# Kernel optimization log

Hardware: AMD Instinct MI355X
Metric: run time of the kernel (lower is better)

Reference implementation:

```python
import jax, jax.numpy as jnp
import numpy as np

IDIM = 512
HDIM = 1024
CDIM = 128  # part_size; topk uses k = 2*CDIM (share=True)
B, T = 16, 4096


def _multihot(idx, n):
    """idx: [B, T, K] int32 -> [B, T, n] float 0/1 multi-hot.
    Matches one_hot(idx, n).float().sum(-2); topk indices are unique so add==set."""
    b, t, k = idx.shape
    rows = jnp.arange(b * t)[:, None]
    m = jnp.zeros((b * t, n), jnp.float32).at[rows, idx.reshape(-1, k)].add(1.0)
    return m.reshape(b, t, n)


def setup_inputs() -> dict:
    key = jax.random.key(0)
    ks = jax.random.split(key, 12)
    inp = {}
    inp["x"] = jax.random.normal(ks[0], (B, T, IDIM), jnp.float32)
    inp["mask_prev"] = (jax.random.uniform(ks[1], (B, T, HDIM)) < 0.1).astype(jnp.float32)

    def lin(k, i, o):
        return jax.random.normal(k, (i, o), jnp.float32) * (1.0 / np.sqrt(i))

    dims_e = [IDIM, 512, 512, 512, HDIM]
    dims_d = [HDIM, 512, 512, 512, IDIM]
    for i in range(4):
        inp[f"e_w{i}"] = lin(ks[2 + i], dims_e[i], dims_e[i + 1])
        inp[f"e_b{i}"] = jnp.zeros((dims_e[i + 1],), jnp.float32)
        inp[f"d_w{i}"] = lin(ks[6 + i], dims_d[i], dims_d[i + 1])
        inp[f"d_b{i}"] = jnp.zeros((dims_d[i + 1],), jnp.float32)
    return inp


def _mlp(x, ws, bs):
    for w, b in zip(ws[:-1], bs[:-1]):
        x = jax.nn.relu(x @ w + b)
    return x @ ws[-1] + bs[-1]


def reference(x, mask_prev,
              e_w0, e_b0, e_w1, e_b1, e_w2, e_b2, e_w3, e_b3,
              d_w0, d_b0, d_w1, d_b1, d_w2, d_b2, d_w3, d_b3):
    h = _mlp(x, [e_w0, e_w1, e_w2, e_w3], [e_b0, e_b1, e_b2, e_b3])  # [B,T,HDIM]

    # hidden_exclude_activation (mask_prev is not None branch)
    h = jnp.where(mask_prev > 0, jnp.float32(0.0), h)  # h[mask_prev.byte()] = 0
    energy = h * h
    _, idx = jax.lax.top_k(energy, 2 * CDIM)            # sorted desc, like torch.topk
    mask_cur_share = _multihot(idx, HDIM)               # top 2*cdim multi-hot
    # h.masked_fill(~mask_cur_share, 0): keep only the shared top-2*cdim energies
    h = h * mask_cur_share

    # decoder
    out = _mlp(h, [d_w0, d_w1, d_w2, d_w3], [d_b0, d_b1, d_b2, d_b3])  # [B,T,IDIM]
    return out
```

## Files before the change

### kernel.cpp

```cpp
#include <hip/hip_runtime.h>

constexpr int NTOK = 16 * 4096;
constexpr int KSEL = 256;
constexpr int UCAP = 8192;

using short8 = __attribute__((ext_vector_type(8))) short;
using f32x4  = __attribute__((ext_vector_type(4))) float;

__device__ inline unsigned short bf16_rne(float x) {
    unsigned u = __float_as_uint(x);
    unsigned r = u + 0x7fffu + ((u >> 16) & 1u);
    return (unsigned short)(r >> 16);
}
__device__ inline float bf16_f32(unsigned short h) {
    return __uint_as_float((unsigned)h << 16);
}

template<int K>
__global__ __launch_bounds__(256)
void gemm_f32(const float* __restrict__ A, const float* __restrict__ W,
              const float* __restrict__ bias, float* __restrict__ C,
              int M, int do_relu, const float* __restrict__ mask)
{
    __shared__ float sA[16][136];
    __shared__ float sW[16][68];

    const int tid = threadIdx.x;
    const int tx = tid & 15, ty = tid >> 4;
    const int rowBase = blockIdx.y * 128;
    const int colBase = blockIdx.x * 64;

    const int lr = tid >> 1;
    const int lk = (tid & 1) * 8;
    const int wk = tid >> 4;
    const int wc = (tid & 15) * 4;

    float acc[8][4] = {};

    for (int k0 = 0; k0 < K; k0 += 16) {
        const float* ap = &A[(size_t)(rowBase + lr) * K + k0 + lk];
        float4 a0 = *(const float4*)ap;
        float4 a1 = *(const float4*)(ap + 4);
        float4 wv = *(const float4*)&W[(size_t)(k0 + wk) * M + colBase + wc];
        __syncthreads();
        sA[lk + 0][lr] = a0.x; sA[lk + 1][lr] = a0.y;
        sA[lk + 2][lr] = a0.z; sA[lk + 3][lr] = a0.w;
        sA[lk + 4][lr] = a1.x; sA[lk + 5][lr] = a1.y;
        sA[lk + 6][lr] = a1.z; sA[lk + 7][lr] = a1.w;
        *(float4*)&sW[wk][wc] = wv;
        __syncthreads();
#pragma unroll
        for (int k = 0; k < 16; ++k) {
            float4 aA = *(const float4*)&sA[k][ty * 8];
            float4 aB = *(const float4*)&sA[k][ty * 8 + 4];
            float4 w4 = *(const float4*)&sW[k][tx * 4];
            float av[8] = {aA.x, aA.y, aA.z, aA.w, aB.x, aB.y, aB.z, aB.w};
            float wl[4] = {w4.x, w4.y, w4.z, w4.w};
#pragma unroll
            for (int a = 0; a < 8; ++a)
#pragma unroll
                for (int b = 0; b < 4; ++b)
                    acc[a][b] = fmaf(av[a], wl[b], acc[a][b]);
        }
    }

    float4 bv = *(const float4*)&bias[colBase + tx * 4];
    float bb[4] = {bv.x, bv.y, bv.z, bv.w};
#pragma unroll
    for (int a = 0; a < 8; ++a) {
        int row = rowBase + ty * 8 + a;
        float o[4];
#pragma unroll
        for (int b = 0; b < 4; ++b) {
            o[b] = acc[a][b] + bb[b];
            if (do_relu) o[b] = fmaxf(o[b], 0.f);
        }
        if (mask) {
            float4 mv = *(const float4*)&mask[(size_t)row * M + colBase + tx * 4];
            float mm[4] = {mv.x, mv.y, mv.z, mv.w};
#pragma unroll
            for (int b = 0; b < 4; ++b) if (mm[b] > 0.f) o[b] = 0.f;
        }
        float4 ov = {o[0], o[1], o[2], o[3]};
        *(float4*)&C[(size_t)row * M + colBase + tx * 4] = ov;
    }
}

__global__ __launch_bounds__(256)
void wsplit_t(const float* __restrict__ W, unsigned short* __restrict__ WhT,
              unsigned short* __restrict__ WlT, int K, int M)
{
    __shared__ float tile[32][33];
    const int tid = threadIdx.x;
    const int tx = tid & 31, ty = tid >> 5;
    const int m0 = blockIdx.x * 32, k0 = blockIdx.y * 32;
#pragma unroll
    for (int i = 0; i < 4; ++i)
        tile[ty + 8 * i][tx] = W[(size_t)(k0 + ty + 8 * i) * M + m0 + tx];
    __syncthreads();
#pragma unroll
    for (int i = 0; i < 4; ++i) {
        int m = ty + 8 * i;
        float v = tile[tx][m];
        unsigned short hh = bf16_rne(v);
        unsigned short ll = bf16_rne(v - bf16_f32(hh));
        WhT[(size_t)(m0 + m) * K + k0 + tx] = hh;
        WlT[(size_t)(m0 + m) * K + k0 + tx] = ll;
    }
}

template<int K>
__global__ __launch_bounds__(256)
void gemm_mfma(const float* __restrict__ A, const unsigned short* __restrict__ WhT,
               const unsigned short* __restrict__ WlT, const float* __restrict__ bias,
               float* __restrict__ C, int M, int do_relu)
{
    __shared__ __align__(16) unsigned short sAh[128 * 40];
    __shared__ __align__(16) unsigned short sAl[128 * 40];
    __shared__ __align__(16) unsigned short sBh[128 * 40];
    __shared__ __align__(16) unsigned short sBl[128 * 40];

    const int tid = threadIdx.x;
    const int lane = tid & 63, wid = tid >> 6;
    const int quad = lane >> 4, l16 = lane & 15;
    const int rowBase = blockIdx.y * 128, colBase = blockIdx.x * 128;
    const int wr = (wid & 1) * 64, wc = (wid >> 1) * 64;

    const int sr = tid >> 1;
    const int sk = (tid & 1) * 16;

    f32x4 acc[4][4];
#pragma unroll
    for (int i = 0; i < 4; ++i)
#pragma unroll
        for (int j = 0; j < 4; ++j)
            acc[i][j] = (f32x4){0.f, 0.f, 0.f, 0.f};

    for (int k0 = 0; k0 < K; k0 += 32) {
        const float* ap = &A[(size_t)(rowBase + sr) * K + k0 + sk];
        float4 a0 = *(const float4*)ap;
        float4 a1 = *(const float4*)(ap + 4);
        float4 a2 = *(const float4*)(ap + 8);
        float4 a3 = *(const float4*)(ap + 12);
        const unsigned short* whp = &WhT[(size_t)(colBase + sr) * K + k0 + sk];
        const unsigned short* wlp = &WlT[(size_t)(colBase + sr) * K + k0 + sk];
        short8 wh0 = *(const short8*)whp;
        short8 wh1 = *(const short8*)(whp + 8);
        short8 wl0 = *(const short8*)wlp;
        short8 wl1 = *(const short8*)(wlp + 8);

        float f[16] = {a0.x, a0.y, a0.z, a0.w, a1.x, a1.y, a1.z, a1.w,
                       a2.x, a2.y, a2.z, a2.w, a3.x, a3.y, a3.z, a3.w};
        unsigned short __align__(16) hs[16], ls[16];
#pragma unroll
        for (int j = 0; j < 16; ++j) {
            hs[j] = bf16_rne(f[j]);
            ls[j] = bf16_rne(f[j] - bf16_f32(hs[j]));
        }

        __syncthreads();
        *(short8*)&sAh[sr * 40 + sk]     = *(short8*)&hs[0];
        *(short8*)&sAh[sr * 40 + sk + 8] = *(short8*)&hs[8];
        *(short8*)&sAl[sr * 40 + sk]     = *(short8*)&ls[0];
        *(short8*)&sAl[sr * 40 + sk + 8] = *(short8*)&ls[8];
        *(short8*)&sBh[sr * 40 + sk]     = wh0;
        *(short8*)&sBh[sr * 40 + sk + 8] = wh1;
        *(short8*)&sBl[sr * 40 + sk]     = wl0;
        *(short8*)&sBl[sr * 40 + sk + 8] = wl1;
        __syncthreads();

        short8 ah[4], al[4], bh[4], bl[4];
#pragma unroll
        for (int t4 = 0; t4 < 4; ++t4) {
            ah[t4] = *(const short8*)&sAh[(wr + t4 * 16 + l16) * 40 + quad * 8];
            al[t4] = *(const short8*)&sAl[(wr + t4 * 16 + l16) * 40 + quad * 8];
            bh[t4] = *(const short8*)&sBh[(wc + t4 * 16 + l16) * 40 + quad * 8];
            bl[t4] = *(const short8*)&sBl[(wc + t4 * 16 + l16) * 40 + quad * 8];
        }
#pragma unroll
        for (int rt = 0; rt < 4; ++rt)
#pragma unroll
            for (int ct = 0; ct < 4; ++ct) {
                acc[rt][ct] = __builtin_amdgcn_mfma_f32_16x16x32_bf16(ah[rt], bh[ct], acc[rt][ct], 0, 0, 0);
                acc[rt][ct] = __builtin_amdgcn_mfma_f32_16x16x32_bf16(al[rt], bh[ct], acc[rt][ct], 0, 0, 0);
                acc[rt][ct] = __builtin_amdgcn_mfma_f32_16x16x32_bf16(ah[rt], bl[ct], acc[rt][ct], 0, 0, 0);
            }
    }

#pragma unroll
    for (int ct = 0; ct < 4; ++ct) {
        int col = colBase + wc + ct * 16 + l16;
        float bc = bias[col];
#pragma unroll
        for (int rt = 0; rt < 4; ++rt)
#pragma unroll
            for (int r = 0; r < 4; ++r) {
                int row = rowBase + wr + rt * 16 + quad * 4 + r;
                float v = acc[rt][ct][r] + bc;
                if (do_relu) v = fmaxf(v, 0.f);
                C[(size_t)row * M + col] = v;
            }
    }
}

__global__ __launch_bounds__(256)
void topk_pass1(float* __restrict__ h, int* __restrict__ meta)
{
    const int t = blockIdx.x, tid = threadIdx.x;
    const int lane = tid & 63, wid = tid >> 6;

    __shared__ unsigned hist[256];
    __shared__ unsigned wsum[4];
    __shared__ unsigned dmx[4];
    __shared__ unsigned s_prefix;
    __shared__ int s_need;

    float4 hv = ((const float4*)(h + (size_t)t * 1024))[tid];
    float v[4] = {hv.x, hv.y, hv.z, hv.w};
    unsigned u[4];
#pragma unroll
    for (int j = 0; j < 4; ++j) u[j] = __float_as_uint(v[j] * v[j]);

    if (tid == 0) { s_prefix = 0u; s_need = KSEL; }
    __syncthreads();

    for (int p = 3; p >= 0; --p) {
        unsigned pref = s_prefix;
        int need = s_need;
        hist[tid] = 0u;
        __syncthreads();
#pragma unroll
        for (int j = 0; j < 4; ++j) {
            bool match = (p == 3) || ((u[j] >> (8 * (p + 1))) == (pref >> (8 * (p + 1))));
            if (match) atomicAdd(&hist[(u[j] >> (8 * p)) & 255u], 1u);
        }
        __syncthreads();
        unsigned x = hist[tid];
        unsigned s = x;
#pragma unroll
        for (int off = 1; off < 64; off <<= 1) {
            unsigned o = __shfl_down(s, off);
            if (lane + off < 64) s += o;
        }
        if (lane == 0) wsum[wid] = s;
        __syncthreads();
        unsigned above = 0;
        for (int w = wid + 1; w < 4; ++w) above += wsum[w];
        unsigned incl = s + above;
        unsigned excl = incl - x;
        if (incl >= (unsigned)need && excl < (unsigned)need) {
            s_prefix = pref | ((unsigned)tid << (8 * p));
            s_need = need - (int)excl;
        }
        __syncthreads();
    }
    const unsigned tau = s_prefix;

    unsigned cg = 0, ce = 0;
#pragma unroll
    for (int j = 0; j < 4; ++j) {
        cg += (u[j] > tau) ? 1u : 0u;
        ce += (u[j] == tau) ? 1u : 0u;
    }
    unsigned packed = (cg << 16) | ce;
    unsigned ps = packed;
#pragma unroll
    for (int off = 1; off < 64; off <<= 1) {
        unsigned o = __shfl_up(ps, off);
        if (lane >= off) ps += o;
    }
    if (lane == 63) wsum[wid] = ps;
    __syncthreads();
    unsigned below = 0;
    for (int w = 0; w < wid; ++w) below += wsum[w];
    unsigned total = wsum[0] + wsum[1] + wsum[2] + wsum[3];
    unsigned incl = ps + below;
    int need_eq = KSEL - (int)(total >> 16);
    int eq_base = (int)((incl - packed) & 0xffffu);

    bool kp[4];
    {
        int r = 0;
#pragma unroll
        for (int j = 0; j < 4; ++j) {
            if (u[j] > tau) kp[j] = true;
            else if (u[j] == tau) { kp[j] = (eq_base + r) < need_eq; ++r; }
            else kp[j] = false;
        }
    }

    unsigned dmax = 0;
#pragma unroll
    for (int j = 0; j < 4; ++j) if (!kp[j] && u[j] > dmax) dmax = u[j];
#pragma unroll
    for (int off = 32; off > 0; off >>= 1) {
        unsigned o = __shfl_xor(dmax, off);
        if (o > dmax) dmax = o;
    }
    if (lane == 0) dmx[wid] = dmax;
    __syncthreads();
    if (tid == 0) {
        unsigned lo = dmx[0];
        for (int w = 1; w < 4; ++w) if (dmx[w] > lo) lo = dmx[w];
        float tauf = __uint_as_float(tau);
        float lof  = __uint_as_float(lo);
        if (tauf - lof <= fmaf(tauf, 1e-4f, 2e-6f)) {
            int slot = atomicAdd(&meta[0], 1);
            if (slot < UCAP) meta[1 + slot] = t;
        }
    }

    float o[4];
#pragma unroll
    for (int j = 0; j < 4; ++j) o[j] = kp[j] ? v[j] : 0.f;
    float4 ov = {o[0], o[1], o[2], o[3]};
    ((float4*)(h + (size_t)t * 1024))[tid] = ov;
}

__global__ __launch_bounds__(256)
void gather_x(const float* __restrict__ x, double* __restrict__ a64,
              const int* __restrict__ meta)
{
    int cnt = meta[0]; if (cnt > UCAP) cnt = UCAP;
    int b = blockIdx.x;
    if (b >= cnt) return;
    int tok = meta[1 + b];
    const float* src = &x[(size_t)tok * 512];
    double* dst = &a64[(size_t)b * 512];
    for (int i = threadIdx.x; i < 512; i += 256) dst[i] = (double)src[i];
}

template<int K, int RELU, int MASKED>
__global__ __launch_bounds__(256)
void gemm_f64(const double* __restrict__ A, const float* __restrict__ W,
              const float* __restrict__ bias, double* __restrict__ Cd,
              int M, const int* __restrict__ meta, const float* __restrict__ mp)
{
    int cnt = meta[0]; if (cnt > UCAP) cnt = UCAP;
    const int rowBase = blockIdx.y * 64;
    if (rowBase >= cnt) return;
    const int colBase = blockIdx.x * 64;

    __shared__ double sA[16][65];
    __shared__ double sW[16][65];
    const int tid = threadIdx.x;
    const int tx = tid & 15, ty = tid >> 4;
    const int lr = tid & 63;
    const int lk4 = (tid >> 6) * 4;
    const int wk = tid >> 4;
    const int wc = (tid & 15) * 4;

    double acc[4][4] = {};

    for (int k0 = 0; k0 < K; k0 += 16) {
        const double* ap = &A[(size_t)(rowBase + lr) * K + k0 + lk4];
        double a0 = ap[0], a1 = ap[1], a2 = ap[2], a3 = ap[3];
        float4 wv = *(const float4*)&W[(size_t)(k0 + wk) * M + colBase + wc];
        __syncthreads();
        sA[lk4 + 0][lr] = a0; sA[lk4 + 1][lr] = a1;
        sA[lk4 + 2][lr] = a2; sA[lk4 + 3][lr] = a3;
        sW[wk][wc + 0] = (double)wv.x; sW[wk][wc + 1] = (double)wv.y;
        sW[wk][wc + 2] = (double)wv.z; sW[wk][wc + 3] = (double)wv.w;
        __syncthreads();
#pragma unroll
        for (int k = 0; k < 16; ++k) {
            double av[4], wl[4];
#pragma unroll
            for (int i = 0; i < 4; ++i) av[i] = sA[k][ty * 4 + i];
#pragma unroll
            for (int i = 0; i < 4; ++i) wl[i] = sW[k][tx * 4 + i];
#pragma unroll
            for (int a = 0; a < 4; ++a)
#pragma unroll
                for (int b = 0; b < 4; ++b)
                    acc[a][b] = fma(av[a], wl[b], acc[a][b]);
        }
    }

#pragma unroll
    for (int a = 0; a < 4; ++a) {
        int row = rowBase + ty * 4 + a;
        if (row >= cnt) continue;
        int tok = MASKED ? meta[1 + row] : 0;
#pragma unroll
        for (int b = 0; b < 4; ++b) {
            int col = colBase + tx * 4 + b;
            double vv = acc[a][b] + (double)bias[col];
            if (RELU) vv = vv > 0.0 ? vv : 0.0;
            if (MASKED) { if (mp[(size_t)tok * 1024 + col] > 0.f) vv = 0.0; }
            Cd[(size_t)row * M + col] = vv;
        }
    }
}

__global__ __launch_bounds__(256)
void topk_pass2(const double* __restrict__ h64, float* __restrict__ h,
                const int* __restrict__ meta)
{
    int cnt = meta[0]; if (cnt > UCAP) cnt = UCAP;
    int b = blockIdx.x;
    if (b >= cnt) return;
    int tok = meta[1 + b];

    __shared__ double se[1024];
    __shared__ unsigned short si[1024];
    __shared__ unsigned char keep[1024];
    const int tid = threadIdx.x;
    const double* row = &h64[(size_t)b * 1024];

#pragma unroll
    for (int t = 0; t < 4; ++t) {
        int i = tid + t * 256;
        double v = row[i];
        se[i] = v * v;
        si[i] = (unsigned short)i;
        keep[i] = 0;
    }
    __syncthreads();

    for (int ksz = 2; ksz <= 1024; ksz <<= 1) {
        for (int j = ksz >> 1; j > 0; j >>= 1) {
#pragma unroll
            for (int t = 0; t < 4; ++t) {
                int i = tid + t * 256;
                int p = i ^ j;
                if (p > i) {
                    double ei = se[i], ep = se[p];
                    unsigned short ii = si[i], ip = si[p];
                    bool later = !((ei > ep) || (ei == ep && ii < ip));
                    bool dir = ((i & ksz) == 0);
                    if (later == dir) {
                        se[i] = ep; se[p] = ei;
                        si[i] = ip; si[p] = ii;
                    }
                }
            }
            __syncthreads();
        }
    }

    keep[si[tid]] = 1;
    __syncthreads();

#pragma unroll
    for (int t = 0; t < 4; ++t) {
        int i = tid + t * 256;
        h[(size_t)tok * 1024 + i] = keep[i] ? (float)row[i] : 0.f;
    }
}

extern "C" void kernel_launch(void* const* d_in, const int* in_sizes, int n_in,
                              void* d_out, int out_size, void* d_ws, size_t ws_size,
                              hipStream_t stream)
{
    (void)n_in; (void)out_size; (void)ws_size;

    const float* x  = (const float*)d_in[0];
    const float* mp = (const float*)d_in[1];

    const float *ew[4], *eb[4], *dw[4], *db[4];
    bool interleaved = (in_sizes[4] == 1024 * 512);
    for (int i = 0; i < 4; ++i) {
        if (interleaved) {
            ew[i] = (const float*)d_in[2 + 4 * i];
            eb[i] = (const float*)d_in[3 + 4 * i];
            dw[i] = (const float*)d_in[4 + 4 * i];
            db[i] = (const float*)d_in[5 + 4 * i];
        } else {
            ew[i] = (const float*)d_in[2 + 2 * i];
            eb[i] = (const float*)d_in[3 + 2 * i];
            dw[i] = (const float*)d_in[10 + 2 * i];
            db[i] = (const float*)d_in[11 + 2 * i];
        }
    }

    float* out  = (float*)d_out;
    float* bufH = (float*)d_ws;
    float* bufP = bufH + (size_t)NTOK * 1024;

    unsigned short* Wh0 = (unsigned short*)d_out;
    unsigned short* Wl0 = Wh0 + 1024 * 512;
    unsigned short* Wh1 = Wl0 + 1024 * 512;
    unsigned short* Wl1 = Wh1 + 512 * 512;
    unsigned short* Wh2 = Wl1 + 512 * 512;
    unsigned short* Wl2 = Wh2 + 512 * 512;
    unsigned short* Wh3 = (unsigned short*)((char*)d_ws + (size_t)192 * 1024 * 1024);
    unsigned short* Wl3 = Wh3 + 512 * 512;

    double* h64 = (double*)((char*)d_out + (size_t)8 * 1024 * 1024);
    int*   meta = (int*)((char*)d_out + (size_t)72 * 1024 * 1024);
    double* a64 = (double*)bufP;
    double* b64 = (double*)((char*)bufP + (size_t)32 * 1024 * 1024);

    dim3 blk(256);

    wsplit_t<<<dim3(512 / 32, 1024 / 32), blk, 0, stream>>>(dw[0], Wh0, Wl0, 1024, 512);
    wsplit_t<<<dim3(512 / 32, 512 / 32),  blk, 0, stream>>>(dw[1], Wh1, Wl1, 512, 512);
    wsplit_t<<<dim3(512 / 32, 512 / 32),  blk, 0, stream>>>(dw[2], Wh2, Wl2, 512, 512);

    dim3 ge(512 / 64, NTOK / 128);
    dim3 ge4(1024 / 64, NTOK / 128);
    gemm_f32<512><<<ge,  blk, 0, stream>>>(x,    ew[0], eb[0], bufP, 512,  1, nullptr);
    gemm_f32<512><<<ge,  blk, 0, stream>>>(bufP, ew[1], eb[1], bufH, 512,  1, nullptr);
    gemm_f32<512><<<ge,  blk, 0, stream>>>(bufH, ew[2], eb[2], bufP, 512,  1, nullptr);
    gemm_f32<512><<<ge4, blk, 0, stream>>>(bufP, ew[3], eb[3], bufH, 1024, 0, mp);

    hipMemsetAsync(meta, 0, sizeof(int), stream);
    topk_pass1<<<dim3(NTOK), blk, 0, stream>>>(bufH, meta);

    dim3 g64a(512 / 64, UCAP / 64), g64b(1024 / 64, UCAP / 64);
    gather_x<<<dim3(UCAP), blk, 0, stream>>>(x, a64, meta);
    gemm_f64<512, 1, 0><<<g64a, blk, 0, stream>>>(a64, ew[0], eb[0], b64, 512,  meta, nullptr);
    gemm_f64<512, 1, 0><<<g64a, blk, 0, stream>>>(b64, ew[1], eb[1], a64, 512,  meta, nullptr);
    gemm_f64<512, 1, 0><<<g64a, blk, 0, stream>>>(a64, ew[2], eb[2], b64, 512,  meta, nullptr);
    gemm_f64<512, 0, 1><<<g64b, blk, 0, stream>>>(b64, ew[3], eb[3], h64, 1024, meta, mp);
    topk_pass2<<<dim3(UCAP), blk, 0, stream>>>(h64, bufH, meta);

    dim3 gd(512 / 128, NTOK / 128);
    gemm_mfma<1024><<<gd, blk, 0, stream>>>(bufH, Wh0, Wl0, db[0], bufP, 512, 1);
    wsplit_t<<<dim3(512 / 32, 512 / 32), blk, 0, stream>>>(dw[3], Wh3, Wl3, 512, 512);
    gemm_mfma<512> <<<gd, blk, 0, stream>>>(bufP, Wh1, Wl1, db[1], bufH, 512, 1);
    gemm_mfma<512> <<<gd, blk, 0, stream>>>(bufH, Wh2, Wl2, db[2], bufP, 512, 1);
    gemm_mfma<512> <<<gd, blk, 0, stream>>>(bufP, Wh3, Wl3, db[3], out,  512, 0);
}
```

Baseline: 4.000 ms.

## Enlarge f32 encoder GEMM tile to 128x128 with 8x8 register blocking and block swizzle

The FP32 encoder GEMM moves from a 128x64 output tile with 8x4 accumulators per thread to a 128x128 tile with 8x8 accumulators per thread. Each thread now reads strided 4-element groups from the low and high halves of shared memory. This roughly doubles arithmetic per shared-memory load and halves the number of A-tile reloads. The kernel also remaps block IDs in groups of eight to improve L2 locality. In exchange it uses more registers per thread, which may lower occupancy, and launches half as many blocks.

```diff
diff --git a/kernel.cpp b/kernel.cpp
--- a/kernel.cpp
+++ b/kernel.cpp
@@ -22,67 +22,82 @@
               const float* __restrict__ bias, float* __restrict__ C,
               int M, int do_relu, const float* __restrict__ mask)
 {
-    __shared__ float sA[16][136];
-    __shared__ float sW[16][68];
+    constexpr int S = 132;
+    __shared__ float sA[16 * S];
+    __shared__ float sW[16 * S];
 
     const int tid = threadIdx.x;
     const int tx = tid & 15, ty = tid >> 4;
-    const int rowBase = blockIdx.y * 128;
-    const int colBase = blockIdx.x * 64;
-
-    const int lr = tid >> 1;
-    const int lk = (tid & 1) * 8;
+
+    const int gridX = gridDim.x;
+    int nwg = gridX * gridDim.y;
+    int bid = blockIdx.y * gridX + blockIdx.x;
+    int cpx = nwg >> 3;
+    int swz = (bid & 7) * cpx + (bid >> 3);
+    const int rowBase = (swz / gridX) * 128;
+    const int colBase = (swz % gridX) * 128;
+
+    const int ar = tid >> 1;
+    const int ak = (tid & 1) * 8;
     const int wk = tid >> 4;
-    const int wc = (tid & 15) * 4;
-
-    float acc[8][4] = {};
+    const int wc = tx * 4;
+
+    float acc[8][8] = {};
 
     for (int k0 = 0; k0 < K; k0 += 16) {
-        const float* ap = &A[(size_t)(rowBase + lr) * K + k0 + lk];
+        const float* ap = &A[(size_t)(rowBase + ar) * K + k0 + ak];
         float4 a0 = *(const float4*)ap;
         float4 a1 = *(const float4*)(ap + 4);
-        float4 wv = *(const float4*)&W[(size_t)(k0 + wk) * M + colBase + wc];
-        __syncthreads();
-        sA[lk + 0][lr] = a0.x; sA[lk + 1][lr] = a0.y;
-        sA[lk + 2][lr] = a0.z; sA[lk + 3][lr] = a0.w;
-        sA[lk + 4][lr] = a1.x; sA[lk + 5][lr] = a1.y;
-        sA[lk + 6][lr] = a1.z; sA[lk + 7][lr] = a1.w;
-        *(float4*)&sW[wk][wc] = wv;
+        const float* wp = &W[(size_t)(k0 + wk) * M + colBase + wc];
+        float4 w0 = *(const float4*)wp;
+        float4 w1 = *(const float4*)(wp + 64);
+        __syncthreads();
+        sA[(ak + 0) * S + ar] = a0.x; sA[(ak + 1) * S + ar] = a0.y;
+        sA[(ak + 2) * S + ar] = a0.z; sA[(ak + 3) * S + ar] = a0.w;
+        sA[(ak + 4) * S + ar] = a1.x; sA[(ak + 5) * S + ar] = a1.y;
+        sA[(ak + 6) * S + ar] = a1.z; sA[(ak + 7) * S + ar] = a1.w;
+        *(float4*)&sW[wk * S + wc]      = w0;
+        *(float4*)&sW[wk * S + wc + 64] = w1;
         __syncthreads();
 #pragma unroll
         for (int k = 0; k < 16; ++k) {
-            float4 aA = *(const float4*)&sA[k][ty * 8];
-            float4 aB = *(const float4*)&sA[k][ty * 8 + 4];
-            float4 w4 = *(const float4*)&sW[k][tx * 4];
-            float av[8] = {aA.x, aA.y, aA.z, aA.w, aB.x, aB.y, aB.z, aB.w};
-            float wl[4] = {w4.x, w4.y, w4.z, w4.w};
-#pragma unroll
-            for (int a = 0; a < 8; ++a)
-#pragma unroll
-                for (int b = 0; b < 4; ++b)
-                    acc[a][b] = fmaf(av[a], wl[b], acc[a][b]);
-        }
-    }
-
-    float4 bv = *(const float4*)&bias[colBase + tx * 4];
-    float bb[4] = {bv.x, bv.y, bv.z, bv.w};
-#pragma unroll
-    for (int a = 0; a < 8; ++a) {
-        int row = rowBase + ty * 8 + a;
-        float o[4];
-#pragma unroll
-        for (int b = 0; b < 4; ++b) {
-            o[b] = acc[a][b] + bb[b];
-            if (do_relu) o[b] = fmaxf(o[b], 0.f);
+            float4 aLo = *(const float4*)&sA[k * S + ty * 4];
+            float4 aHi = *(const float4*)&sA[k * S + 64 + ty * 4];
+            float4 wLo = *(const float4*)&sW[k * S + tx * 4];
+            float4 wHi = *(const float4*)&sW[k * S + 64 + tx * 4];
+            float av[8] = {aLo.x, aLo.y, aLo.z, aLo.w, aHi.x, aHi.y, aHi.z, aHi.w};
+            float wv[8] = {wLo.x, wLo.y, wLo.z, wLo.w, wHi.x, wHi.y, wHi.z, wHi.w};
+#pragma unroll
+            for (int i = 0; i < 8; ++i)
+#pragma unroll
+                for (int j = 0; j < 8; ++j)
+                    acc[i][j] = fmaf(av[i], wv[j], acc[i][j]);
+        }
+    }
+
+    float4 b0 = *(const float4*)&bias[colBase + tx * 4];
+    float4 b1 = *(const float4*)&bias[colBase + 64 + tx * 4];
+    float bb[8] = {b0.x, b0.y, b0.z, b0.w, b1.x, b1.y, b1.z, b1.w};
+#pragma unroll
+    for (int i = 0; i < 8; ++i) {
+        int row = rowBase + ((i < 4) ? (ty * 4 + i) : (64 + ty * 4 + (i - 4)));
+        float o[8];
+#pragma unroll
+        for (int j = 0; j < 8; ++j) {
+            o[j] = acc[i][j] + bb[j];
+            if (do_relu) o[j] = fmaxf(o[j], 0.f);
         }
         if (mask) {
-            float4 mv = *(const float4*)&mask[(size_t)row * M + colBase + tx * 4];
-            float mm[4] = {mv.x, mv.y, mv.z, mv.w};
-#pragma unroll
-            for (int b = 0; b < 4; ++b) if (mm[b] > 0.f) o[b] = 0.f;
-        }
-        float4 ov = {o[0], o[1], o[2], o[3]};
-        *(float4*)&C[(size_t)row * M + colBase + tx * 4] = ov;
+            float4 m0 = *(const float4*)&mask[(size_t)row * M + colBase + tx * 4];
+            float4 m1 = *(const float4*)&mask[(size_t)row * M + colBase + 64 + tx * 4];
+            float mm[8] = {m0.x, m0.y, m0.z, m0.w, m1.x, m1.y, m1.z, m1.w};
+#pragma unroll
+            for (int j = 0; j < 8; ++j) if (mm[j] > 0.f) o[j] = 0.f;
+        }
+        float4 v0 = {o[0], o[1], o[2], o[3]};
+        float4 v1 = {o[4], o[5], o[6], o[7]};
+        *(float4*)&C[(size_t)row * M + colBase + tx * 4]      = v0;
+        *(float4*)&C[(size_t)row * M + colBase + 64 + tx * 4] = v1;
     }
 }
 
@@ -498,8 +513,8 @@
     wsplit_t<<<dim3(512 / 32, 512 / 32),  blk, 0, stream>>>(dw[1], Wh1, Wl1, 512, 512);
     wsplit_t<<<dim3(512 / 32, 512 / 32),  blk, 0, stream>>>(dw[2], Wh2, Wl2, 512, 512);
 
-    dim3 ge(512 / 64, NTOK / 128);
-    dim3 ge4(1024 / 64, NTOK / 128);
+    dim3 ge(512 / 128, NTOK / 128);
+    dim3 ge4(1024 / 128, NTOK / 128);
     gemm_f32<512><<<ge,  blk, 0, stream>>>(x,    ew[0], eb[0], bufP, 512,  1, nullptr);
     gemm_f32<512><<<ge,  blk, 0, stream>>>(bufP, ew[1], eb[1], bufH, 512,  1, nullptr);
     gemm_f32<512><<<ge,  blk, 0, stream>>>(bufH, ew[2], eb[2], bufP, 512,  1, nullptr);
```

Result: faster. 3.653 ms (-8.7%).
